# Kernel optimization log

Measured on AMD Instinct MI355X. Metric: run time of the kernel, lower is better.

## Reference

```python
import jax, jax.numpy as jnp
import numpy as np

B, N, E = 256, 4096, 65536  # graphs, nodes/graph (64*64), edges/graph


def setup_inputs() -> dict:
    key = jax.random.key(0)
    k = jax.random.split(key, 6)
    x = jax.random.normal(k[0], (B, N, 3), dtype=jnp.float32)
    src = jax.random.randint(k[1], (E,), 0, N, dtype=jnp.int32)
    dst = jax.random.randint(k[2], (E,), 0, N, dtype=jnp.int32)
    W1 = jax.random.normal(k[3], (3, 64), dtype=jnp.float32) * 0.3
    b1 = jnp.zeros((64,), dtype=jnp.float32)
    Wfc = jax.random.normal(k[4], (N * 64, 1), dtype=jnp.float32) * 0.002
    bfc = jnp.zeros((1,), dtype=jnp.float32)
    return {"x": x, "W1": W1, "b1": b1, "Wfc": Wfc, "bfc": bfc,
            "src": src, "dst": dst}


def reference(x, W1, b1, Wfc, bfc, src, dst):
    # DGL GraphConv, norm='both': h = relu(D_in^{-1/2} A D_out^{-1/2} x W + b)
    ones = jnp.ones((E,), dtype=x.dtype)
    deg_out = jax.ops.segment_sum(ones, src, num_segments=N)
    deg_in = jax.ops.segment_sum(ones, dst, num_segments=N)
    c_src = jax.lax.rsqrt(jnp.maximum(deg_out, 1.0))  # [N]
    c_dst = jax.lax.rsqrt(jnp.maximum(deg_in, 1.0))   # [N]
    # gather normalized source features, scatter-add into destinations
    msg = (x * c_src[None, :, None])[:, src]          # [B, E, 3]
    agg = jnp.zeros_like(x).at[:, dst].add(msg)       # [B, N, 3]
    h = jax.nn.relu((agg * c_dst[None, :, None]) @ W1 + b1)  # [B, N, 64]
    # fc: flatten per graph, Linear(N*64 -> 1) + sigmoid
    logits = h.reshape(x.shape[0], -1) @ Wfc + bfc    # [B, 1]
    return jax.nn.sigmoid(logits)
```

## Files before the change

### kernel.cpp

```cpp
#include <hip/hip_runtime.h>
#include <math.h>

#define Bg 256
#define Nn 4096
#define Ee 65536
#define Kk (Nn * 3)

__global__ __launch_bounds__(256) void k_degrees(const int* __restrict__ src,
                                                 const int* __restrict__ dst,
                                                 int* __restrict__ deg_out,
                                                 int* __restrict__ deg_in) {
    int e = blockIdx.x * 256 + threadIdx.x;
    if (e < Ee) {
        atomicAdd(&deg_out[src[e]], 1);
        atomicAdd(&deg_in[dst[e]], 1);
    }
}

__global__ __launch_bounds__(256) void k_norm_scan(const int* __restrict__ deg_out,
                                                   const int* __restrict__ deg_in,
                                                   float* __restrict__ c_src,
                                                   float* __restrict__ c_dst,
                                                   int* __restrict__ row_ptr) {
    int t = threadIdx.x;
    int base = t * 16;
    int local[16];
    int s = 0;
#pragma unroll
    for (int i = 0; i < 16; i++) {
        int di = deg_in[base + i];
        local[i] = di;
        s += di;
        c_dst[base + i] = rsqrtf(fmaxf((float)di, 1.0f));
        int dq = deg_out[base + i];
        c_src[base + i] = rsqrtf(fmaxf((float)dq, 1.0f));
    }
    int lane = t & 63, w = t >> 6;
    int inc = s;
#pragma unroll
    for (int d = 1; d < 64; d <<= 1) {
        int v = __shfl_up(inc, d, 64);
        if (lane >= d) inc += v;
    }
    __shared__ int wtot[4], woff[4];
    if (lane == 63) wtot[w] = inc;
    __syncthreads();
    if (t == 0) { int run = 0; for (int i = 0; i < 4; i++) { woff[i] = run; run += wtot[i]; } }
    __syncthreads();
    int run = inc - s + woff[w];
#pragma unroll
    for (int i = 0; i < 16; i++) { row_ptr[base + i] = run; run += local[i]; }
    if (t == 255) row_ptr[Nn] = run;
}

__global__ __launch_bounds__(256) void k_fill(const int* __restrict__ src,
                                              const int* __restrict__ dst,
                                              const int* __restrict__ row_ptr,
                                              int* __restrict__ cursor,
                                              int* __restrict__ csr_src) {
    int e = blockIdx.x * 256 + threadIdx.x;
    if (e < Ee) {
        int d = dst[e];
        int ofs = atomicAdd(&cursor[d], 1);
        csr_src[row_ptr[d] + ofs] = src[e];
    }
}

__global__ __launch_bounds__(256) void k_transpose(const float* __restrict__ x,
                                                   const float* __restrict__ c_src,
                                                   float* __restrict__ xs2) {
    __shared__ float4 tile4[64][49];
    int t = threadIdx.x;
    int n0 = blockIdx.x * 64;
    int bq = blockIdx.y;
    const float* xb = x + (size_t)bq * 64 * Kk + (size_t)n0 * 3;
#pragma unroll
    for (int i = 0; i < 12; i++) {
        int idx = i * 256 + t;
        int bi = idx / 48, j = idx - bi * 48;
        tile4[bi][j] = ((const float4*)(xb + (size_t)bi * Kk))[j];
    }
    __syncthreads();
    const float* tile = (const float*)tile4;
    float4* outp = (float4*)(xs2 + (size_t)bq * (Nn * 192) + (size_t)n0 * 192);
#pragma unroll
    for (int i = 0; i < 12; i++) {
        int o4 = i * 256 + t;
        int nn = o4 / 48, q = o4 - nn * 48;
        int f0 = q * 4;
        float cs = c_src[n0 + nn];
        float4 v;
        {
            int f = f0;     int bl = f / 3, c = f - 3 * bl; v.x = tile[bl * 196 + nn * 3 + c];
        }
        {
            int f = f0 + 1; int bl = f / 3, c = f - 3 * bl; v.y = tile[bl * 196 + nn * 3 + c];
        }
        {
            int f = f0 + 2; int bl = f / 3, c = f - 3 * bl; v.z = tile[bl * 196 + nn * 3 + c];
        }
        {
            int f = f0 + 3; int bl = f / 3, c = f - 3 * bl; v.w = tile[bl * 196 + nn * 3 + c];
        }
        v.x *= cs; v.y *= cs; v.z *= cs; v.w *= cs;
        outp[o4] = v;
    }
}

__global__ __launch_bounds__(256, 6) void k_main(const float* __restrict__ xs2,
                                                 const float* __restrict__ W1,
                                                 const float* __restrict__ b1,
                                                 const float* __restrict__ Wfc,
                                                 const float* __restrict__ c_dst,
                                                 const int* __restrict__ row_ptr,
                                                 const int* __restrict__ csr_src,
                                                 float* __restrict__ partial) {
    __shared__ float4 sW14[64];
    __shared__ float sWfc[4][64];
    __shared__ float red[4][64];
    int t = threadIdx.x & 63;
    int w = threadIdx.x >> 6;
    int bq = blockIdx.x & 3;
    int g  = blockIdx.x >> 2;
    int n  = g * 4 + w;
    if (w == 0) sW14[t] = make_float4(W1[t], W1[64 + t], W1[128 + t], b1[t]);
    sWfc[w][t] = Wfc[n * 64 + t];
    __syncthreads();

    const float* slab = xs2 + (size_t)bq * (Nn * 192);
    int s0 = row_ptr[n], s1 = row_ptr[n + 1];
    int vt = t * 3;
    float a0 = 0.f, a1 = 0.f, a2 = 0.f;
    int i = s0;
    for (; i + 4 <= s1; i += 4) {
        const float* p0 = slab + csr_src[i]     * 192 + vt;
        const float* p1 = slab + csr_src[i + 1] * 192 + vt;
        const float* p2 = slab + csr_src[i + 2] * 192 + vt;
        const float* p3 = slab + csr_src[i + 3] * 192 + vt;
        float u0 = p0[0], u1 = p0[1], u2 = p0[2];
        float v0 = p1[0], v1 = p1[1], v2 = p1[2];
        float w0 = p2[0], w1 = p2[1], w2 = p2[2];
        float z0 = p3[0], z1 = p3[1], z2 = p3[2];
        a0 += (u0 + v0) + (w0 + z0);
        a1 += (u1 + v1) + (w1 + z1);
        a2 += (u2 + v2) + (w2 + z2);
    }
    for (; i < s1; i++) {
        const float* p = slab + csr_src[i] * 192 + vt;
        a0 += p[0]; a1 += p[1]; a2 += p[2];
    }
    float cd = c_dst[n];
    a0 *= cd; a1 *= cd; a2 *= cd;

    float part = 0.f;
#pragma unroll 8
    for (int f = 0; f < 64; f++) {
        float4 wv = sW14[f];
        float h = fmaf(a0, wv.x, fmaf(a1, wv.y, fmaf(a2, wv.z, wv.w)));
        part = fmaf(fmaxf(h, 0.f), sWfc[w][f], part);
    }
    red[w][t] = part;
    __syncthreads();
    if (w == 0) {
        float tot = (red[0][t] + red[1][t]) + (red[2][t] + red[3][t]);
        partial[(size_t)g * 256 + bq * 64 + t] = tot;
    }
}

__global__ __launch_bounds__(256) void k_reduce(const float* __restrict__ partial,
                                                float* __restrict__ out_acc,
                                                int chunk) {
    int t = threadIdx.x;
    int g0 = blockIdx.x * chunk;
    float s = 0.f;
    for (int g = 0; g < chunk; g++) s += partial[(size_t)(g0 + g) * 256 + t];
    atomicAdd(&out_acc[t], s);
}

__global__ __launch_bounds__(256) void k_final(const float* __restrict__ out_acc,
                                               const float* __restrict__ bfc,
                                               float* __restrict__ out) {
    int t = threadIdx.x;
    float v = out_acc[t] + bfc[0];
    out[t] = 1.0f / (1.0f + expf(-v));
}

extern "C" void kernel_launch(void* const* d_in, const int* in_sizes, int n_in,
                              void* d_out, int out_size, void* d_ws, size_t ws_size,
                              hipStream_t stream) {
    const float* x   = (const float*)d_in[0];
    const float* W1  = (const float*)d_in[1];
    const float* b1  = (const float*)d_in[2];
    const float* Wfc = (const float*)d_in[3];
    const float* bfc = (const float*)d_in[4];
    const int*   src = (const int*)d_in[5];
    const int*   dst = (const int*)d_in[6];
    float* out = (float*)d_out;

    char* ws = (char*)d_ws;
    float* xs2 = (float*)ws;
    const size_t Z = (size_t)Kk * Bg * 4;
    int*   deg_out = (int*)(ws + Z);
    int*   deg_in  = (int*)(ws + Z + 16384);
    int*   cursor  = (int*)(ws + Z + 32768);
    float* out_acc = (float*)(ws + Z + 49152);
    float* c_src   = (float*)(ws + Z + 50176);
    float* c_dst   = (float*)(ws + Z + 66560);
    int*   row_ptr = (int*)(ws + Z + 82944);
    int*   csr_src = (int*)(ws + Z + 99344);
    float* partial = (float*)(ws + Z + 361488);

    hipMemsetAsync(ws + Z, 0, 50176, stream);
    k_degrees<<<Ee / 256, 256, 0, stream>>>(src, dst, deg_out, deg_in);
    k_norm_scan<<<1, 256, 0, stream>>>(deg_out, deg_in, c_src, c_dst, row_ptr);
    k_fill<<<Ee / 256, 256, 0, stream>>>(src, dst, row_ptr, cursor, csr_src);
    k_transpose<<<dim3(Nn / 64, 4), 256, 0, stream>>>(x, c_src, xs2);
    k_main<<<1024 * 4, 256, 0, stream>>>(xs2, W1, b1, Wfc, c_dst, row_ptr, csr_src, partial);
    k_reduce<<<64, 256, 0, stream>>>(partial, out_acc, 16);
    k_final<<<1, 256, 0, stream>>>(out_acc, bfc, out);
}
```

Before: 126.0 us.

## Store normalized features as packed bf16 and fuse partial reduction via atomics

The transposed, source-normalized feature buffer is now stored as bf16 triples packed into uint2 (8 bytes per node per graph instead of 12). Each thread fetches one aligned 8-byte load per edge, and the gather loop is unrolled to 8 edges with two accumulator sets for more memory-level parallelism. The separate partial-sum buffer and reduce kernel are replaced by direct atomicAdd into the output accumulator, which removes one launch and one global round trip. The trade-off is reduced precision of the gathered features and more contended atomics on 256 addresses.

```diff
diff --git a/kernel.cpp b/kernel.cpp
--- a/kernel.cpp
+++ b/kernel.cpp
@@ -5,6 +5,11 @@
 #define Nn 4096
 #define Ee 65536
 #define Kk (Nn * 3)
+
+__device__ __forceinline__ unsigned bf16r(float v) {
+    unsigned b = __float_as_uint(v);
+    return (b + 0x7fffu + ((b >> 16) & 1u)) >> 16;
+}
 
 __global__ __launch_bounds__(256) void k_degrees(const int* __restrict__ src,
                                                  const int* __restrict__ dst,
@@ -68,7 +73,7 @@
 
 __global__ __launch_bounds__(256) void k_transpose(const float* __restrict__ x,
                                                    const float* __restrict__ c_src,
-                                                   float* __restrict__ xs2) {
+                                                   uint2* __restrict__ xsb) {
     __shared__ float4 tile4[64][49];
     int t = threadIdx.x;
     int n0 = blockIdx.x * 64;
@@ -82,39 +87,30 @@
     }
     __syncthreads();
     const float* tile = (const float*)tile4;
-    float4* outp = (float4*)(xs2 + (size_t)bq * (Nn * 192) + (size_t)n0 * 192);
-#pragma unroll
-    for (int i = 0; i < 12; i++) {
-        int o4 = i * 256 + t;
-        int nn = o4 / 48, q = o4 - nn * 48;
-        int f0 = q * 4;
+    uint2* outp = xsb + ((size_t)bq * Nn + n0) * 64;
+#pragma unroll
+    for (int i = 0; i < 16; i++) {
+        int idx = i * 256 + t;
+        int nn = idx >> 6, bl = idx & 63;
         float cs = c_src[n0 + nn];
-        float4 v;
-        {
-            int f = f0;     int bl = f / 3, c = f - 3 * bl; v.x = tile[bl * 196 + nn * 3 + c];
-        }
-        {
-            int f = f0 + 1; int bl = f / 3, c = f - 3 * bl; v.y = tile[bl * 196 + nn * 3 + c];
-        }
-        {
-            int f = f0 + 2; int bl = f / 3, c = f - 3 * bl; v.z = tile[bl * 196 + nn * 3 + c];
-        }
-        {
-            int f = f0 + 3; int bl = f / 3, c = f - 3 * bl; v.w = tile[bl * 196 + nn * 3 + c];
-        }
-        v.x *= cs; v.y *= cs; v.z *= cs; v.w *= cs;
-        outp[o4] = v;
-    }
-}
-
-__global__ __launch_bounds__(256, 6) void k_main(const float* __restrict__ xs2,
-                                                 const float* __restrict__ W1,
-                                                 const float* __restrict__ b1,
-                                                 const float* __restrict__ Wfc,
-                                                 const float* __restrict__ c_dst,
-                                                 const int* __restrict__ row_ptr,
-                                                 const int* __restrict__ csr_src,
-                                                 float* __restrict__ partial) {
+        float f0 = tile[bl * 196 + nn * 3 + 0] * cs;
+        float f1 = tile[bl * 196 + nn * 3 + 1] * cs;
+        float f2 = tile[bl * 196 + nn * 3 + 2] * cs;
+        uint2 u;
+        u.x = bf16r(f0) | (bf16r(f1) << 16);
+        u.y = bf16r(f2);
+        outp[(size_t)nn * 64 + bl] = u;
+    }
+}
+
+__global__ __launch_bounds__(256) void k_main(const uint2* __restrict__ xsb,
+                                              const float* __restrict__ W1,
+                                              const float* __restrict__ b1,
+                                              const float* __restrict__ Wfc,
+                                              const float* __restrict__ c_dst,
+                                              const int* __restrict__ row_ptr,
+                                              const int* __restrict__ csr_src,
+                                              float* __restrict__ out_acc) {
     __shared__ float4 sW14[64];
     __shared__ float sWfc[4][64];
     __shared__ float red[4][64];
@@ -127,28 +123,36 @@
     sWfc[w][t] = Wfc[n * 64 + t];
     __syncthreads();
 
-    const float* slab = xs2 + (size_t)bq * (Nn * 192);
+    const uint2* slab = xsb + (size_t)bq * (Nn * 64);
     int s0 = row_ptr[n], s1 = row_ptr[n + 1];
-    int vt = t * 3;
     float a0 = 0.f, a1 = 0.f, a2 = 0.f;
+    float c0 = 0.f, c1 = 0.f, c2 = 0.f;
     int i = s0;
-    for (; i + 4 <= s1; i += 4) {
-        const float* p0 = slab + csr_src[i]     * 192 + vt;
-        const float* p1 = slab + csr_src[i + 1] * 192 + vt;
-        const float* p2 = slab + csr_src[i + 2] * 192 + vt;
-        const float* p3 = slab + csr_src[i + 3] * 192 + vt;
-        float u0 = p0[0], u1 = p0[1], u2 = p0[2];
-        float v0 = p1[0], v1 = p1[1], v2 = p1[2];
-        float w0 = p2[0], w1 = p2[1], w2 = p2[2];
-        float z0 = p3[0], z1 = p3[1], z2 = p3[2];
-        a0 += (u0 + v0) + (w0 + z0);
-        a1 += (u1 + v1) + (w1 + z1);
-        a2 += (u2 + v2) + (w2 + z2);
+    for (; i + 8 <= s1; i += 8) {
+        uint2 u0 = slab[(csr_src[i + 0] << 6) + t];
+        uint2 u1 = slab[(csr_src[i + 1] << 6) + t];
+        uint2 u2 = slab[(csr_src[i + 2] << 6) + t];
+        uint2 u3 = slab[(csr_src[i + 3] << 6) + t];
+        uint2 u4 = slab[(csr_src[i + 4] << 6) + t];
+        uint2 u5 = slab[(csr_src[i + 5] << 6) + t];
+        uint2 u6 = slab[(csr_src[i + 6] << 6) + t];
+        uint2 u7 = slab[(csr_src[i + 7] << 6) + t];
+        a0 += __uint_as_float(u0.x << 16); a1 += __uint_as_float(u0.x & 0xffff0000u); a2 += __uint_as_float(u0.y << 16);
+        c0 += __uint_as_float(u1.x << 16); c1 += __uint_as_float(u1.x & 0xffff0000u); c2 += __uint_as_float(u1.y << 16);
+        a0 += __uint_as_float(u2.x << 16); a1 += __uint_as_float(u2.x & 0xffff0000u); a2 += __uint_as_float(u2.y << 16);
+        c0 += __uint_as_float(u3.x << 16); c1 += __uint_as_float(u3.x & 0xffff0000u); c2 += __uint_as_float(u3.y << 16);
+        a0 += __uint_as_float(u4.x << 16); a1 += __uint_as_float(u4.x & 0xffff0000u); a2 += __uint_as_float(u4.y << 16);
+        c0 += __uint_as_float(u5.x << 16); c1 += __uint_as_float(u5.x & 0xffff0000u); c2 += __uint_as_float(u5.y << 16);
+        a0 += __uint_as_float(u6.x << 16); a1 += __uint_as_float(u6.x & 0xffff0000u); a2 += __uint_as_float(u6.y << 16);
+        c0 += __uint_as_float(u7.x << 16); c1 += __uint_as_float(u7.x & 0xffff0000u); c2 += __uint_as_float(u7.y << 16);
     }
     for (; i < s1; i++) {
-        const float* p = slab + csr_src[i] * 192 + vt;
-        a0 += p[0]; a1 += p[1]; a2 += p[2];
-    }
+        uint2 u = slab[(csr_src[i] << 6) + t];
+        a0 += __uint_as_float(u.x << 16);
+        a1 += __uint_as_float(u.x & 0xffff0000u);
+        a2 += __uint_as_float(u.y << 16);
+    }
+    a0 += c0; a1 += c1; a2 += c2;
     float cd = c_dst[n];
     a0 *= cd; a1 *= cd; a2 *= cd;
 
@@ -163,18 +167,8 @@
     __syncthreads();
     if (w == 0) {
         float tot = (red[0][t] + red[1][t]) + (red[2][t] + red[3][t]);
-        partial[(size_t)g * 256 + bq * 64 + t] = tot;
-    }
-}
-
-__global__ __launch_bounds__(256) void k_reduce(const float* __restrict__ partial,
-                                                float* __restrict__ out_acc,
-                                                int chunk) {
-    int t = threadIdx.x;
-    int g0 = blockIdx.x * chunk;
-    float s = 0.f;
-    for (int g = 0; g < chunk; g++) s += partial[(size_t)(g0 + g) * 256 + t];
-    atomicAdd(&out_acc[t], s);
+        atomicAdd(&out_acc[bq * 64 + t], tot);
+    }
 }
 
 __global__ __launch_bounds__(256) void k_final(const float* __restrict__ out_acc,
@@ -198,8 +192,8 @@
     float* out = (float*)d_out;
 
     char* ws = (char*)d_ws;
-    float* xs2 = (float*)ws;
-    const size_t Z = (size_t)Kk * Bg * 4;
+    uint2* xsb = (uint2*)ws;
+    const size_t Z = (size_t)4 * Nn * 64 * 8;
     int*   deg_out = (int*)(ws + Z);
     int*   deg_in  = (int*)(ws + Z + 16384);
     int*   cursor  = (int*)(ws + Z + 32768);
@@ -208,14 +202,12 @@
     float* c_dst   = (float*)(ws + Z + 66560);
     int*   row_ptr = (int*)(ws + Z + 82944);
     int*   csr_src = (int*)(ws + Z + 99344);
-    float* partial = (float*)(ws + Z + 361488);
 
     hipMemsetAsync(ws + Z, 0, 50176, stream);
     k_degrees<<<Ee / 256, 256, 0, stream>>>(src, dst, deg_out, deg_in);
     k_norm_scan<<<1, 256, 0, stream>>>(deg_out, deg_in, c_src, c_dst, row_ptr);
     k_fill<<<Ee / 256, 256, 0, stream>>>(src, dst, row_ptr, cursor, csr_src);
-    k_transpose<<<dim3(Nn / 64, 4), 256, 0, stream>>>(x, c_src, xs2);
-    k_main<<<1024 * 4, 256, 0, stream>>>(xs2, W1, b1, Wfc, c_dst, row_ptr, csr_src, partial);
-    k_reduce<<<64, 256, 0, stream>>>(partial, out_acc, 16);
+    k_transpose<<<dim3(Nn / 64, 4), 256, 0, stream>>>(x, c_src, xsb);
+    k_main<<<1024 * 4, 256, 0, stream>>>(xsb, W1, b1, Wfc, c_dst, row_ptr, csr_src, out_acc);
     k_final<<<1, 256, 0, stream>>>(out_acc, bfc, out);
 }
```

After: 136.5 us. +8.4%, slower.
